# Kernel optimization log

Hardware: AMD Instinct MI355X
Metric: run time of the kernel (lower is better)

## Reference

```python
import jax, jax.numpy as jnp
import numpy as np

B, S, D, H = 4, 1024, 1024, 16
DH = D // H  # 64, per-head dim; FFN hidden = 2048
DFF = 2048

def setup_inputs() -> dict:
    key = jax.random.key(0)
    ks = jax.random.split(key, 6)
    x = jax.random.normal(ks[0], (B, S, D), dtype=jnp.float32)
    # Per-head q/k/v projection weights, stacked over heads: [H, D, DH].
    # Equivalent math to n_heads separate SelfAttentionLayer(d_head) calls + concat.
    sc_in = 1.0 / np.sqrt(D)
    Wq = jax.random.normal(ks[1], (H, D, DH), dtype=jnp.float32) * sc_in
    Wk = jax.random.normal(ks[2], (H, D, DH), dtype=jnp.float32) * sc_in
    Wv = jax.random.normal(ks[3], (H, D, DH), dtype=jnp.float32) * sc_in
    W1 = jax.random.normal(ks[4], (D, DFF), dtype=jnp.float32) * sc_in
    b1 = jnp.zeros((DFF,), dtype=jnp.float32)
    W2 = jax.random.normal(ks[5], (DFF, D), dtype=jnp.float32) * (1.0 / np.sqrt(DFF))
    b2 = jnp.zeros((D,), dtype=jnp.float32)
    return {"x": x, "Wq": Wq, "Wk": Wk, "Wv": Wv,
            "W1": W1, "b1": b1, "W2": W2, "b2": b2}

def reference(x, Wq, Wk, Wv, W1, b1, W2, b2):
    # Batched multi-head self-attention (math-equivalent to the per-head loop + concat).
    q = jnp.einsum('bsd,hde->bhse', x, Wq)          # [B,H,S,DH]
    k = jnp.einsum('bsd,hde->bhse', x, Wk)
    v = jnp.einsum('bsd,hde->bhse', x, Wv)
    scale = 1.0 / jnp.sqrt(jnp.asarray(q.shape[-1], q.dtype))
    scores = jnp.einsum('bhqe,bhke->bhqk', q, k) * scale  # [B,H,S,S]
    attn = jax.nn.softmax(scores, axis=-1)
    o = jnp.einsum('bhqk,bhke->bhqe', attn, v)      # [B,H,S,DH]
    h1 = o.transpose(0, 2, 1, 3).reshape(x.shape[0], x.shape[1], -1)  # concat heads -> [B,S,D]
    # FCLayer(2048, d): Dense(2048, relu) -> Dense(d)
    y = jax.nn.relu(h1 @ W1 + b1) @ W2 + b2
    return y
```

## Files before the change

### kernel.cpp

```cpp
#include <hip/hip_runtime.h>
#include <hip/hip_bf16.h>


typedef unsigned short u16;
typedef __attribute__((ext_vector_type(8))) short bfrag8;
typedef __attribute__((ext_vector_type(4))) float f32x4;
typedef __attribute__((ext_vector_type(16))) float f32x16;
typedef __attribute__((ext_vector_type(4))) int ix4;

constexpr int Bb = 4, Ss = 1024, Dd = 1024, Hh = 16, DFF = 2048;
constexpr float QSCALE = 0.18033688011112042f;

__device__ __forceinline__ u16 f2bf(float f) {
  unsigned u = __float_as_uint(f);
  return (u16)((u + 0x7fffu + ((u >> 16) & 1u)) >> 16);
}

__device__ __forceinline__ void gload16(const void* g, void* l) {
  __builtin_amdgcn_global_load_lds(
      (const __attribute__((address_space(1))) unsigned int*)g,
      (__attribute__((address_space(3))) unsigned int*)l, 16, 0, 0);
}

__device__ __forceinline__ int xcd_swz() {
  const int id = blockIdx.y * gridDim.x + blockIdx.x;
  const int cpx = (gridDim.x * gridDim.y) >> 3;
  return (id & 7) * cpx + (id >> 3);
}

__global__ __launch_bounds__(256) void cvt_bf16(const float* __restrict__ in,
                                                u16* __restrict__ out, int n4) {
  int i = blockIdx.x * 256 + threadIdx.x;
  if (i >= n4) return;
  float4 v = ((const float4*)in)[i];
  ushort4 o = make_ushort4(f2bf(v.x), f2bf(v.y), f2bf(v.z), f2bf(v.w));
  *(ushort4*)(out + (size_t)i * 4) = o;
}

__device__ __forceinline__ void transpose64(const float* __restrict__ in,
                                            u16* __restrict__ out,
                                            int R, int C, int r0, int c0) {
  __shared__ float tile[64][65];
  const int t = threadIdx.x, cl = t & 63, rq = t >> 6;
#pragma unroll
  for (int i = 0; i < 16; ++i) {
    int rl = rq * 16 + i;
    tile[rl][cl] = in[(size_t)(r0 + rl) * C + c0 + cl];
  }
  __syncthreads();
#pragma unroll
  for (int i = 0; i < 16; ++i) {
    int oc = rq * 16 + i;
    out[(size_t)(c0 + oc) * R + r0 + cl] = f2bf(tile[cl][oc]);
  }
}

__global__ __launch_bounds__(256) void transpose_cvt(const float* __restrict__ in,
                                                     u16* __restrict__ out,
                                                     int R, int C) {
  transpose64(in, out, R, C, blockIdx.x * 64, blockIdx.y * 64);
}

__global__ __launch_bounds__(256) void qkv_transpose_cvt(
    const float* __restrict__ Wq, const float* __restrict__ Wk,
    const float* __restrict__ Wv, u16* __restrict__ out) {
  const int z = blockIdx.y;
  const int which = z >> 4, h = z & 15;
  const float* in = (which == 0 ? Wq : which == 1 ? Wk : Wv) + (size_t)h * 1024 * 64;
  u16* o = out + (size_t)z * 64 * 1024;
  transpose64(in, o, 1024, 64, blockIdx.x * 64, 0);
}

template <int EPI>
__global__ __launch_bounds__(256) void mfma_gemm(
    const u16* __restrict__ A, const u16* __restrict__ Bt,
    const float* __restrict__ bias, void* __restrict__ Cout, int N, int K) {
  __shared__ alignas(16) u16 Asm[128 * 32];
  __shared__ alignas(16) u16 Bsm[128 * 32];
  const int tid = threadIdx.x;
  const int wid = tid >> 6, lane = tid & 63;
  const int nid = xcd_swz();
  const int m0 = (nid / gridDim.x) * 128, n0 = (nid % gridDim.x) * 128;
  const int wr = wid >> 1, wc = wid & 1;
  const int fr = lane & 15, krow = lane >> 4;

  const int srow = tid >> 2;
  const int sk = (tid & 3) * 8;
  const u16* ga0 = A + (size_t)(m0 + srow) * K + sk;
  const u16* ga1 = A + (size_t)(m0 + srow + 64) * K + sk;
  const u16* gb0 = Bt + (size_t)(n0 + srow) * K + sk;
  const u16* gb1 = Bt + (size_t)(n0 + srow + 64) * K + sk;
  char* lA0 = (char*)Asm + tid * 16;
  char* lA1 = lA0 + 4096;
  char* lB0 = (char*)Bsm + tid * 16;
  char* lB1 = lB0 + 4096;

  f32x4 acc[4][4];
#pragma unroll
  for (int i = 0; i < 4; ++i)
#pragma unroll
    for (int j = 0; j < 4; ++j) acc[i][j] = (f32x4){0.f, 0.f, 0.f, 0.f};

  const char* pa = (const char*)Asm + (wr * 64 + fr) * 64 + krow * 16;
  const char* pb = (const char*)Bsm + (wc * 64 + fr) * 64 + krow * 16;

  for (int kt = 0; kt < K / 32; ++kt) {
    __syncthreads();
    gload16(ga0 + kt * 32, lA0);
    gload16(ga1 + kt * 32, lA1);
    gload16(gb0 + kt * 32, lB0);
    gload16(gb1 + kt * 32, lB1);
    __syncthreads();

    bfrag8 af[4], bfv[4];
#pragma unroll
    for (int i = 0; i < 4; ++i) af[i] = *(const bfrag8*)(pa + i * 1024);
#pragma unroll
    for (int j = 0; j < 4; ++j) bfv[j] = *(const bfrag8*)(pb + j * 1024);
#pragma unroll
    for (int i = 0; i < 4; ++i)
#pragma unroll
      for (int j = 0; j < 4; ++j)
        acc[i][j] = __builtin_amdgcn_mfma_f32_16x16x32_bf16(af[i], bfv[j], acc[i][j], 0, 0, 0);
  }

  const int orow = (lane >> 4) * 4;
  const int ocol = lane & 15;
#pragma unroll
  for (int i = 0; i < 4; ++i) {
#pragma unroll
    for (int j = 0; j < 4; ++j) {
      const int gn = n0 + wc * 64 + j * 16 + ocol;
      const int gm0 = m0 + wr * 64 + i * 16 + orow;
      if (EPI == 0) {
        const int which = gn >> 10, hh = (gn >> 6) & 15, e = gn & 63;
        const int bb = gm0 >> 10, s0 = gm0 & 1023;
        const int hb = hh * 4 + bb;
        u16* oq = (u16*)Cout;
        if (which == 0) {
#pragma unroll
          for (int r = 0; r < 4; ++r)
            oq[((size_t)hb * 1024 + s0 + r) * 64 + e] = f2bf(acc[i][j][r] * QSCALE);
        } else if (which == 1) {
#pragma unroll
          for (int r = 0; r < 4; ++r)
            oq[4194304 + ((size_t)hb * 1024 + s0 + r) * 64 + e] = f2bf(acc[i][j][r]);
        } else {
          ushort4 pk = make_ushort4(f2bf(acc[i][j][0]), f2bf(acc[i][j][1]),
                                    f2bf(acc[i][j][2]), f2bf(acc[i][j][3]));
          *(ushort4*)&oq[8388608 + ((size_t)hb * 64 + e) * 1024 + s0] = pk;
        }
      } else if (EPI == 1) {
#pragma unroll
        for (int r = 0; r < 4; ++r) {
          float v = fmaxf(acc[i][j][r] + bias[gn], 0.f);
          ((u16*)Cout)[(size_t)(gm0 + r) * N + gn] = f2bf(v);
        }
      } else {
#pragma unroll
        for (int r = 0; r < 4; ++r)
          ((float*)Cout)[(size_t)(gm0 + r) * N + gn] = acc[i][j][r] + bias[gn];
      }
    }
  }
}

__global__ __launch_bounds__(256) void mfma_gemm_n64(
    const u16* __restrict__ A, const u16* __restrict__ Bt,
    const float* __restrict__ bias, float* __restrict__ Cout, int N, int K) {
  __shared__ alignas(16) u16 Asm[128 * 32];
  __shared__ alignas(16) u16 Bsm[64 * 32];
  const int tid = threadIdx.x;
  const int wid = tid >> 6, lane = tid & 63;
  const int nid = xcd_swz();
  const int m0 = (nid / gridDim.x) * 128, n0 = (nid % gridDim.x) * 64;
  const int fr = lane & 15, krow = lane >> 4;

  const int srow = tid >> 2;
  const int sk = (tid & 3) * 8;
  const u16* ga0 = A + (size_t)(m0 + srow) * K + sk;
  const u16* ga1 = A + (size_t)(m0 + srow + 64) * K + sk;
  const u16* gb0 = Bt + (size_t)(n0 + srow) * K + sk;
  char* lA0 = (char*)Asm + tid * 16;
  char* lA1 = lA0 + 4096;
  char* lB0 = (char*)Bsm + tid * 16;

  f32x4 acc[2][4];
#pragma unroll
  for (int i = 0; i < 2; ++i)
#pragma unroll
    for (int j = 0; j < 4; ++j) acc[i][j] = (f32x4){0.f, 0.f, 0.f, 0.f};

  const char* pa = (const char*)Asm + (wid * 32 + fr) * 64 + krow * 16;
  const char* pb = (const char*)Bsm + fr * 64 + krow * 16;

  for (int kt = 0; kt < K / 32; ++kt) {
    __syncthreads();
    gload16(ga0 + kt * 32, lA0);
    gload16(ga1 + kt * 32, lA1);
    gload16(gb0 + kt * 32, lB0);
    __syncthreads();

    bfrag8 af[2], bfv[4];
#pragma unroll
    for (int i = 0; i < 2; ++i) af[i] = *(const bfrag8*)(pa + i * 1024);
#pragma unroll
    for (int j = 0; j < 4; ++j) bfv[j] = *(const bfrag8*)(pb + j * 1024);
#pragma unroll
    for (int i = 0; i < 2; ++i)
#pragma unroll
      for (int j = 0; j < 4; ++j)
        acc[i][j] = __builtin_amdgcn_mfma_f32_16x16x32_bf16(af[i], bfv[j], acc[i][j], 0, 0, 0);
  }

  const int orow = (lane >> 4) * 4;
  const int ocol = lane & 15;
#pragma unroll
  for (int i = 0; i < 2; ++i)
#pragma unroll
    for (int j = 0; j < 4; ++j) {
      const int gn = n0 + j * 16 + ocol;
      const int gm0 = m0 + wid * 32 + i * 16 + orow;
#pragma unroll
      for (int r = 0; r < 4; ++r)
        Cout[(size_t)(gm0 + r) * N + gn] = acc[i][j][r] + bias[gn];
    }
}

__global__ __launch_bounds__(256, 2) void attn_mfma32(
    const u16* __restrict__ qb, const u16* __restrict__ kb,
    const u16* __restrict__ vtb, u16* __restrict__ h1) {
  const int wid = threadIdx.x >> 6, lane = threadIdx.x & 63;
  const int nid = xcd_swz();
  const int qx = nid & 7, hb = nid >> 3;
  const int h = hb >> 2, b = hb & 3;
  const int q0 = qx * 128 + wid * 32;
  const int ql = lane & 31, hi = lane >> 5;

  const u16* Qp  = qb + ((size_t)hb * 1024 + q0 + ql) * 64 + hi * 8;
  const u16* Kp0 = kb + (size_t)hb * 65536 + (size_t)ql * 64 + hi * 8;
  const u16* Kp1 = Kp0 + 32 * 64;
  const u16* Vp0 = vtb + (size_t)hb * 65536 + (size_t)ql * 1024 + hi * 8;
  const u16* Vp1 = Vp0 + 32 * 1024;

  bfrag8 qf[4];
#pragma unroll
  for (int st = 0; st < 4; ++st) qf[st] = *(const bfrag8*)(Qp + st * 16);

  f32x16 po0, po1;
#pragma unroll
  for (int i = 0; i < 16; ++i) { po0[i] = 0.f; po1[i] = 0.f; }
  float mrun = -1e30f, lrun = 0.f;

#define PACK4(dst, p, base)                                                    \
  {                                                                            \
    int a0, a1, b0, b1;                                                        \
    asm("v_cvt_pk_bf16_f32 %0, %1, %2" : "=v"(a0)                              \
        : "v"(p[base + 0]), "v"(p[base + 1]));                                 \
    asm("v_cvt_pk_bf16_f32 %0, %1, %2" : "=v"(a1)                              \
        : "v"(p[base + 2]), "v"(p[base + 3]));                                 \
    asm("v_cvt_pk_bf16_f32 %0, %1, %2" : "=v"(b0)                              \
        : "v"(p[base + 4]), "v"(p[base + 5]));                                 \
    asm("v_cvt_pk_bf16_f32 %0, %1, %2" : "=v"(b1)                              \
        : "v"(p[base + 6]), "v"(p[base + 7]));                                 \
    asm("v_permlane32_swap_b32 %0, %1" : "+v"(a0), "+v"(b0));                  \
    asm("v_permlane32_swap_b32 %0, %1" : "+v"(a1), "+v"(b1));                  \
    ix4 t = (ix4){a0, a1, b0, b1};                                             \
    dst = __builtin_bit_cast(bfrag8, t);                                       \
  }

  for (int kt = 0; kt < 16; ++kt) {
    const u16* k0 = Kp0 + kt * 4096;
    const u16* k1 = Kp1 + kt * 4096;
    const u16* v0 = Vp0 + kt * 64;
    const u16* v1 = Vp1 + kt * 64;
    bfrag8 kf0[4], kf1[4], vf0[4], vf1[4];
#pragma unroll
    for (int st = 0; st < 4; ++st) {
      kf0[st] = *(const bfrag8*)(k0 + st * 16);
      kf1[st] = *(const bfrag8*)(k1 + st * 16);
      vf0[st] = *(const bfrag8*)(v0 + st * 16);
      vf1[st] = *(const bfrag8*)(v1 + st * 16);
    }

    f32x16 pa0, pa1;
#pragma unroll
    for (int i = 0; i < 16; ++i) { pa0[i] = 0.f; pa1[i] = 0.f; }
    __builtin_amdgcn_s_setprio(1);
#pragma unroll
    for (int st = 0; st < 4; ++st) {
      pa0 = __builtin_amdgcn_mfma_f32_32x32x16_bf16(kf0[st], qf[st], pa0, 0, 0, 0);
      pa1 = __builtin_amdgcn_mfma_f32_32x32x16_bf16(kf1[st], qf[st], pa1, 0, 0, 0);
    }
    __builtin_amdgcn_s_setprio(0);

    float cm = fmaxf(pa0[0], pa1[0]);
#pragma unroll
    for (int i = 1; i < 16; ++i) cm = fmaxf(cm, fmaxf(pa0[i], pa1[i]));
    cm = fmaxf(cm, __shfl_xor(cm, 32));
    const float mnew = fmaxf(mrun, cm);
    const float scl = exp2f(mrun - mnew);
    mrun = mnew;
    float psum = 0.f;
#pragma unroll
    for (int i = 0; i < 16; ++i) {
      pa0[i] = exp2f(pa0[i] - mnew);
      pa1[i] = exp2f(pa1[i] - mnew);
      psum += pa0[i] + pa1[i];
    }
    psum += __shfl_xor(psum, 32);
    lrun = lrun * scl + psum;
    po0 *= scl;
    po1 *= scl;

    bfrag8 pf00, pf01, pf10, pf11;
    PACK4(pf00, pa0, 0);
    PACK4(pf01, pa0, 8);
    PACK4(pf10, pa1, 0);
    PACK4(pf11, pa1, 8);

    __builtin_amdgcn_s_setprio(1);
    po0 = __builtin_amdgcn_mfma_f32_32x32x16_bf16(vf0[0], pf00, po0, 0, 0, 0);
    po0 = __builtin_amdgcn_mfma_f32_32x32x16_bf16(vf0[1], pf01, po0, 0, 0, 0);
    po0 = __builtin_amdgcn_mfma_f32_32x32x16_bf16(vf0[2], pf10, po0, 0, 0, 0);
    po0 = __builtin_amdgcn_mfma_f32_32x32x16_bf16(vf0[3], pf11, po0, 0, 0, 0);
    po1 = __builtin_amdgcn_mfma_f32_32x32x16_bf16(vf1[0], pf00, po1, 0, 0, 0);
    po1 = __builtin_amdgcn_mfma_f32_32x32x16_bf16(vf1[1], pf01, po1, 0, 0, 0);
    po1 = __builtin_amdgcn_mfma_f32_32x32x16_bf16(vf1[2], pf10, po1, 0, 0, 0);
    po1 = __builtin_amdgcn_mfma_f32_32x32x16_bf16(vf1[3], pf11, po1, 0, 0, 0);
    __builtin_amdgcn_s_setprio(0);
  }
#undef PACK4

  const float inv = 1.f / lrun;
  u16* orow = h1 + ((size_t)(b * 1024 + q0 + ql)) * 1024 + h * 64 + hi * 4;
#pragma unroll
  for (int r4 = 0; r4 < 4; ++r4) {
    ushort4 o0 = make_ushort4(
        f2bf(po0[r4 * 4 + 0] * inv), f2bf(po0[r4 * 4 + 1] * inv),
        f2bf(po0[r4 * 4 + 2] * inv), f2bf(po0[r4 * 4 + 3] * inv));
    *(ushort4*)(orow + r4 * 8) = o0;
    ushort4 o1 = make_ushort4(
        f2bf(po1[r4 * 4 + 0] * inv), f2bf(po1[r4 * 4 + 1] * inv),
        f2bf(po1[r4 * 4 + 2] * inv), f2bf(po1[r4 * 4 + 3] * inv));
    *(ushort4*)(orow + 32 + r4 * 8) = o1;
  }
}

extern "C" void kernel_launch(void* const* d_in, const int* in_sizes, int n_in,
                              void* d_out, int out_size, void* d_ws, size_t ws_size,
                              hipStream_t stream) {
  const float* x  = (const float*)d_in[0];
  const float* Wq = (const float*)d_in[1];
  const float* Wk = (const float*)d_in[2];
  const float* Wv = (const float*)d_in[3];
  const float* W1 = (const float*)d_in[4];
  const float* b1 = (const float*)d_in[5];
  const float* W2 = (const float*)d_in[6];
  const float* b2 = (const float*)d_in[7];

  const size_t MB = 1u << 20;
  char* w = (char*)d_ws;
  u16* qkvb  = (u16*)w;
  u16* Xb    = (u16*)(w + 24 * MB);
  u16* Wqkvt = (u16*)(w + 32 * MB);
  u16* W1t   = (u16*)(w + 38 * MB);
  u16* W2t   = (u16*)(w + 42 * MB);
  u16* h1b   = (u16*)(w + 46 * MB);
  u16* ffb   = (u16*)(w + 54 * MB);

  cvt_bf16<<<4096, 256, 0, stream>>>(x, Xb, 1048576);
  qkv_transpose_cvt<<<dim3(16, 48), 256, 0, stream>>>(Wq, Wk, Wv, Wqkvt);
  transpose_cvt<<<dim3(16, 32), 256, 0, stream>>>(W1, W1t, 1024, 2048);
  transpose_cvt<<<dim3(32, 16), 256, 0, stream>>>(W2, W2t, 2048, 1024);

  mfma_gemm<0><<<dim3(24, 32), 256, 0, stream>>>(Xb, Wqkvt, nullptr, qkvb, 3072, 1024);
  attn_mfma32<<<dim3(8, 64), 256, 0, stream>>>(qkvb, qkvb + 4194304, qkvb + 8388608, h1b);
  mfma_gemm<1><<<dim3(16, 32), 256, 0, stream>>>(h1b, W1t, b1, ffb, 2048, 1024);
  mfma_gemm_n64<<<dim3(16, 32), 256, 0, stream>>>(ffb, W2t, b2, (float*)d_out, 1024, 2048);
}
```

Before: 275.1 us.

## Double-buffer K/V loads in attention, lazy softmax rescale, separate V transpose

Result: no change. 269.8 us (-1.9%).

```diff
diff --git a/kernel.cpp b/kernel.cpp
--- a/kernel.cpp
+++ b/kernel.cpp
@@ -69,6 +69,26 @@
   const float* in = (which == 0 ? Wq : which == 1 ? Wk : Wv) + (size_t)h * 1024 * 64;
   u16* o = out + (size_t)z * 64 * 1024;
   transpose64(in, o, 1024, 64, blockIdx.x * 64, 0);
+}
+
+__global__ __launch_bounds__(256) void vt_transpose(const u16* __restrict__ in,
+                                                    u16* __restrict__ out) {
+  __shared__ float tile[64][65];
+  const int hb = blockIdx.y, s0 = blockIdx.x * 64;
+  const int t = threadIdx.x, cl = t & 63, rq = t >> 6;
+#pragma unroll
+  for (int i = 0; i < 16; ++i) {
+    const int rl = rq * 16 + i;
+    tile[rl][cl] = __uint_as_float(
+        (unsigned)in[((size_t)hb * 1024 + s0 + rl) * 64 + cl] << 16);
+  }
+  __syncthreads();
+#pragma unroll
+  for (int i = 0; i < 16; ++i) {
+    const int oc = rq * 16 + i;
+    out[((size_t)hb * 64 + oc) * 1024 + s0 + cl] =
+        (u16)(__float_as_uint(tile[cl][oc]) >> 16);
+  }
 }
 
 template <int EPI>
@@ -136,20 +156,11 @@
         const int which = gn >> 10, hh = (gn >> 6) & 15, e = gn & 63;
         const int bb = gm0 >> 10, s0 = gm0 & 1023;
         const int hb = hh * 4 + bb;
-        u16* oq = (u16*)Cout;
-        if (which == 0) {
-#pragma unroll
-          for (int r = 0; r < 4; ++r)
-            oq[((size_t)hb * 1024 + s0 + r) * 64 + e] = f2bf(acc[i][j][r] * QSCALE);
-        } else if (which == 1) {
-#pragma unroll
-          for (int r = 0; r < 4; ++r)
-            oq[4194304 + ((size_t)hb * 1024 + s0 + r) * 64 + e] = f2bf(acc[i][j][r]);
-        } else {
-          ushort4 pk = make_ushort4(f2bf(acc[i][j][0]), f2bf(acc[i][j][1]),
-                                    f2bf(acc[i][j][2]), f2bf(acc[i][j][3]));
-          *(ushort4*)&oq[8388608 + ((size_t)hb * 64 + e) * 1024 + s0] = pk;
-        }
+        u16* oq = (u16*)Cout + (size_t)which * 4194304 +
+                  ((size_t)hb * 1024 + s0) * 64 + e;
+        const float sc = (which == 0) ? QSCALE : 1.f;
+#pragma unroll
+        for (int r = 0; r < 4; ++r) oq[r * 64] = f2bf(acc[i][j][r] * sc);
       } else if (EPI == 1) {
 #pragma unroll
         for (int r = 0; r < 4; ++r) {
@@ -237,11 +248,9 @@
   const int q0 = qx * 128 + wid * 32;
   const int ql = lane & 31, hi = lane >> 5;
 
-  const u16* Qp  = qb + ((size_t)hb * 1024 + q0 + ql) * 64 + hi * 8;
-  const u16* Kp0 = kb + (size_t)hb * 65536 + (size_t)ql * 64 + hi * 8;
-  const u16* Kp1 = Kp0 + 32 * 64;
-  const u16* Vp0 = vtb + (size_t)hb * 65536 + (size_t)ql * 1024 + hi * 8;
-  const u16* Vp1 = Vp0 + 32 * 1024;
+  const u16* Qp = qb + ((size_t)hb * 1024 + q0 + ql) * 64 + hi * 8;
+  const u16* Kp = kb + (size_t)hb * 65536 + (size_t)ql * 64 + hi * 8;
+  const u16* Vp = vtb + (size_t)hb * 65536 + (size_t)ql * 1024 + hi * 8;
 
   bfrag8 qf[4];
 #pragma unroll
@@ -251,6 +260,23 @@
 #pragma unroll
   for (int i = 0; i < 16; ++i) { po0[i] = 0.f; po1[i] = 0.f; }
   float mrun = -1e30f, lrun = 0.f;
+
+  bfrag8 kA[8], kB[8], vv[8];
+
+#define LOADK(dst, kt)                                                         \
+  {                                                                            \
+    _Pragma("unroll") for (int st = 0; st < 4; ++st) {                         \
+      dst[st]     = *(const bfrag8*)(Kp + (size_t)(kt) * 4096 + st * 16);      \
+      dst[4 + st] = *(const bfrag8*)(Kp + (size_t)(kt) * 4096 + 2048 + st * 16); \
+    }                                                                          \
+  }
+#define LOADV(dst, kt)                                                         \
+  {                                                                            \
+    _Pragma("unroll") for (int st = 0; st < 4; ++st) {                         \
+      dst[st]     = *(const bfrag8*)(Vp + (kt) * 64 + st * 16);                \
+      dst[4 + st] = *(const bfrag8*)(Vp + 32768 + (kt) * 64 + st * 16);        \
+    }                                                                          \
+  }
 
 #define PACK4(dst, p, base)                                                    \
   {                                                                            \
@@ -269,68 +295,77 @@
     dst = __builtin_bit_cast(bfrag8, t);                                       \
   }
 
-  for (int kt = 0; kt < 16; ++kt) {
-    const u16* k0 = Kp0 + kt * 4096;
-    const u16* k1 = Kp1 + kt * 4096;
-    const u16* v0 = Vp0 + kt * 64;
-    const u16* v1 = Vp1 + kt * 64;
-    bfrag8 kf0[4], kf1[4], vf0[4], vf1[4];
-#pragma unroll
-    for (int st = 0; st < 4; ++st) {
-      kf0[st] = *(const bfrag8*)(k0 + st * 16);
-      kf1[st] = *(const bfrag8*)(k1 + st * 16);
-      vf0[st] = *(const bfrag8*)(v0 + st * 16);
-      vf1[st] = *(const bfrag8*)(v1 + st * 16);
-    }
-
-    f32x16 pa0, pa1;
-#pragma unroll
-    for (int i = 0; i < 16; ++i) { pa0[i] = 0.f; pa1[i] = 0.f; }
-    __builtin_amdgcn_s_setprio(1);
-#pragma unroll
-    for (int st = 0; st < 4; ++st) {
-      pa0 = __builtin_amdgcn_mfma_f32_32x32x16_bf16(kf0[st], qf[st], pa0, 0, 0, 0);
-      pa1 = __builtin_amdgcn_mfma_f32_32x32x16_bf16(kf1[st], qf[st], pa1, 0, 0, 0);
-    }
-    __builtin_amdgcn_s_setprio(0);
-
-    float cm = fmaxf(pa0[0], pa1[0]);
-#pragma unroll
-    for (int i = 1; i < 16; ++i) cm = fmaxf(cm, fmaxf(pa0[i], pa1[i]));
-    cm = fmaxf(cm, __shfl_xor(cm, 32));
-    const float mnew = fmaxf(mrun, cm);
-    const float scl = exp2f(mrun - mnew);
-    mrun = mnew;
-    float psum = 0.f;
-#pragma unroll
-    for (int i = 0; i < 16; ++i) {
-      pa0[i] = exp2f(pa0[i] - mnew);
-      pa1[i] = exp2f(pa1[i] - mnew);
-      psum += pa0[i] + pa1[i];
-    }
-    psum += __shfl_xor(psum, 32);
-    lrun = lrun * scl + psum;
-    po0 *= scl;
-    po1 *= scl;
-
-    bfrag8 pf00, pf01, pf10, pf11;
-    PACK4(pf00, pa0, 0);
-    PACK4(pf01, pa0, 8);
-    PACK4(pf10, pa1, 0);
-    PACK4(pf11, pa1, 8);
-
-    __builtin_amdgcn_s_setprio(1);
-    po0 = __builtin_amdgcn_mfma_f32_32x32x16_bf16(vf0[0], pf00, po0, 0, 0, 0);
-    po0 = __builtin_amdgcn_mfma_f32_32x32x16_bf16(vf0[1], pf01, po0, 0, 0, 0);
-    po0 = __builtin_amdgcn_mfma_f32_32x32x16_bf16(vf0[2], pf10, po0, 0, 0, 0);
-    po0 = __builtin_amdgcn_mfma_f32_32x32x16_bf16(vf0[3], pf11, po0, 0, 0, 0);
-    po1 = __builtin_amdgcn_mfma_f32_32x32x16_bf16(vf1[0], pf00, po1, 0, 0, 0);
-    po1 = __builtin_amdgcn_mfma_f32_32x32x16_bf16(vf1[1], pf01, po1, 0, 0, 0);
-    po1 = __builtin_amdgcn_mfma_f32_32x32x16_bf16(vf1[2], pf10, po1, 0, 0, 0);
-    po1 = __builtin_amdgcn_mfma_f32_32x32x16_bf16(vf1[3], pf11, po1, 0, 0, 0);
-    __builtin_amdgcn_s_setprio(0);
-  }
+#define STEP(kf)                                                               \
+  {                                                                            \
+    f32x16 pa0, pa1;                                                           \
+    _Pragma("unroll") for (int i = 0; i < 16; ++i) { pa0[i] = 0.f; pa1[i] = 0.f; } \
+    __builtin_amdgcn_s_setprio(1);                                             \
+    _Pragma("unroll") for (int st = 0; st < 4; ++st) {                         \
+      pa0 = __builtin_amdgcn_mfma_f32_32x32x16_bf16(kf[st], qf[st], pa0, 0, 0, 0); \
+      pa1 = __builtin_amdgcn_mfma_f32_32x32x16_bf16(kf[4 + st], qf[st], pa1, 0, 0, 0); \
+    }                                                                          \
+    __builtin_amdgcn_s_setprio(0);                                             \
+    float t4[8];                                                               \
+    _Pragma("unroll") for (int g = 0; g < 4; ++g) {                            \
+      t4[g] = fmaxf(fmaxf(pa0[4 * g], pa0[4 * g + 1]),                         \
+                    fmaxf(pa0[4 * g + 2], pa0[4 * g + 3]));                    \
+      t4[4 + g] = fmaxf(fmaxf(pa1[4 * g], pa1[4 * g + 1]),                     \
+                        fmaxf(pa1[4 * g + 2], pa1[4 * g + 3]));                \
+    }                                                                          \
+    float cm = fmaxf(fmaxf(fmaxf(t4[0], t4[1]), fmaxf(t4[2], t4[3])),          \
+                     fmaxf(fmaxf(t4[4], t4[5]), fmaxf(t4[6], t4[7])));         \
+    cm = fmaxf(cm, __shfl_xor(cm, 32));                                        \
+    if (__any(cm > mrun + 8.f)) {    \
+      const float mnew = fmaxf(mrun, cm);                                      \
+      const float scl = exp2f(mrun - mnew);                                    \
+      mrun = mnew;                                                             \
+      lrun *= scl;                                                             \
+      po0 *= scl;                                                              \
+      po1 *= scl;                                                              \
+    }                                                                          \
+    _Pragma("unroll") for (int i = 0; i < 16; ++i) {                           \
+      pa0[i] = exp2f(pa0[i] - mrun);                                           \
+      pa1[i] = exp2f(pa1[i] - mrun);                                           \
+    }                                                                          \
+    float s4[8];                                                               \
+    _Pragma("unroll") for (int g = 0; g < 4; ++g) {                            \
+      s4[g] = (pa0[4 * g] + pa0[4 * g + 1]) + (pa0[4 * g + 2] + pa0[4 * g + 3]); \
+      s4[4 + g] = (pa1[4 * g] + pa1[4 * g + 1]) + (pa1[4 * g + 2] + pa1[4 * g + 3]); \
+    }                                                                          \
+    float psum = ((s4[0] + s4[1]) + (s4[2] + s4[3])) +                         \
+                 ((s4[4] + s4[5]) + (s4[6] + s4[7]));                          \
+    psum += __shfl_xor(psum, 32);                                              \
+    lrun += psum;                                                              \
+    bfrag8 pf00, pf01, pf10, pf11;                                             \
+    PACK4(pf00, pa0, 0);                                                       \
+    PACK4(pf01, pa0, 8);                                                       \
+    PACK4(pf10, pa1, 0);                                                       \
+    PACK4(pf11, pa1, 8);                                                       \
+    __builtin_amdgcn_s_setprio(1);                                             \
+    po0 = __builtin_amdgcn_mfma_f32_32x32x16_bf16(vv[0], pf00, po0, 0, 0, 0);  \
+    po0 = __builtin_amdgcn_mfma_f32_32x32x16_bf16(vv[1], pf01, po0, 0, 0, 0);  \
+    po0 = __builtin_amdgcn_mfma_f32_32x32x16_bf16(vv[2], pf10, po0, 0, 0, 0);  \
+    po0 = __builtin_amdgcn_mfma_f32_32x32x16_bf16(vv[3], pf11, po0, 0, 0, 0);  \
+    po1 = __builtin_amdgcn_mfma_f32_32x32x16_bf16(vv[4], pf00, po1, 0, 0, 0);  \
+    po1 = __builtin_amdgcn_mfma_f32_32x32x16_bf16(vv[5], pf01, po1, 0, 0, 0);  \
+    po1 = __builtin_amdgcn_mfma_f32_32x32x16_bf16(vv[6], pf10, po1, 0, 0, 0);  \
+    po1 = __builtin_amdgcn_mfma_f32_32x32x16_bf16(vv[7], pf11, po1, 0, 0, 0);  \
+    __builtin_amdgcn_s_setprio(0);                                             \
+  }
+
+  LOADK(kA, 0);
+  for (int kt = 0; kt < 16; kt += 2) {
+    LOADV(vv, kt);
+    LOADK(kB, kt + 1);
+    STEP(kA);
+    LOADV(vv, kt + 1);
+    if (kt + 2 < 16) LOADK(kA, kt + 2);
+    STEP(kB);
+  }
+#undef LOADK
+#undef LOADV
 #undef PACK4
+#undef STEP
 
   const float inv = 1.f / lrun;
   u16* orow = h1 + ((size_t)(b * 1024 + q0 + ql)) * 1024 + h * 64 + hi * 4;
@@ -362,12 +397,13 @@
   const size_t MB = 1u << 20;
   char* w = (char*)d_ws;
   u16* qkvb  = (u16*)w;
-  u16* Xb    = (u16*)(w + 24 * MB);
-  u16* Wqkvt = (u16*)(w + 32 * MB);
-  u16* W1t   = (u16*)(w + 38 * MB);
-  u16* W2t   = (u16*)(w + 42 * MB);
-  u16* h1b   = (u16*)(w + 46 * MB);
-  u16* ffb   = (u16*)(w + 54 * MB);
+  u16* vtb   = (u16*)(w + 24 * MB);
+  u16* Xb    = (u16*)(w + 32 * MB);
+  u16* Wqkvt = (u16*)(w + 40 * MB);
+  u16* W1t   = (u16*)(w + 46 * MB);
+  u16* W2t   = (u16*)(w + 50 * MB);
+  u16* h1b   = (u16*)(w + 54 * MB);
+  u16* ffb   = (u16*)(w + 62 * MB);
 
   cvt_bf16<<<4096, 256, 0, stream>>>(x, Xb, 1048576);
   qkv_transpose_cvt<<<dim3(16, 48), 256, 0, stream>>>(Wq, Wk, Wv, Wqkvt);
@@ -375,7 +411,8 @@
   transpose_cvt<<<dim3(32, 16), 256, 0, stream>>>(W2, W2t, 2048, 1024);
 
   mfma_gemm<0><<<dim3(24, 32), 256, 0, stream>>>(Xb, Wqkvt, nullptr, qkvb, 3072, 1024);
-  attn_mfma32<<<dim3(8, 64), 256, 0, stream>>>(qkvb, qkvb + 4194304, qkvb + 8388608, h1b);
+  vt_transpose<<<dim3(16, 64), 256, 0, stream>>>(qkvb + 8388608, vtb);
+  attn_mfma32<<<dim3(8, 64), 256, 0, stream>>>(qkvb, qkvb + 4194304, vtb, h1b);
   mfma_gemm<1><<<dim3(16, 32), 256, 0, stream>>>(h1b, W1t, b1, ffb, 2048, 1024);
   mfma_gemm_n64<<<dim3(16, 32), 256, 0, stream>>>(ffb, W2t, b2, (float*)d_out, 1024, 2048);
 }
```
